# Performance work log

Measured on AMD Instinct MI355X. Metric: run time of the kernel, lower is better.

Reference implementation:

```python
import jax, jax.numpy as jnp
from jax import lax
import numpy as np

B, T, H, L = 4096, 7, 512, 256
D = 2 * H  # bidirectional LSTM feature dim


def _lstm(x, wih, whh, bih, bhh, reverse):
    # x: [B, T, L]; torch gate order i, f, g, o
    b, hdim = x.shape[0], whh.shape[0]
    xs = jnp.swapaxes(x, 0, 1)  # [T, B, L]
    bias = bih + bhh

    def step(carry, xt):
        h, c = carry
        gates = xt @ wih + h @ whh + bias
        i, f, g, o = jnp.split(gates, 4, axis=-1)
        c = jax.nn.sigmoid(f) * c + jax.nn.sigmoid(i) * jnp.tanh(g)
        h = jax.nn.sigmoid(o) * jnp.tanh(c)
        return (h, c), h

    h0 = jnp.zeros((b, hdim), x.dtype)
    _, hs = lax.scan(step, (h0, h0), xs, reverse=reverse)
    return jnp.swapaxes(hs, 0, 1)  # [B, T, H]


def _att(enc, dec):
    # Sequential attention: keys/values start as enc and grow with each decoder output.
    keys = enc  # [B, T, D]
    outs = []
    for i in range(dec.shape[1]):  # fixed small T=7, Python loop is static
        q = dec[:, i, :]                                  # [B, D]
        scores = jnp.einsum('bd,btd->bt', q, keys)        # dot over features
        a = jax.nn.softmax(scores, axis=1)
        ctx = jnp.einsum('bt,btd->bd', a, keys)
        out = ctx + q
        outs.append(out)
        keys = jnp.concatenate([keys, out[:, None, :]], axis=1)
    return jnp.stack(outs, axis=1)  # [B, T, D]


def _deconv(x, w, b):
    # torch ConvTranspose2d (stride 1, pad 0) == full conv with flipped, in/out-swapped kernel
    kh, kw = w.shape[2], w.shape[3]
    w2 = jnp.transpose(w[:, :, ::-1, ::-1], (1, 0, 2, 3))  # [out, in, kh, kw]
    y = lax.conv_general_dilated(x, w2, (1, 1), ((kh - 1, kh - 1), (kw - 1, kw - 1)),
                                 dimension_numbers=('NCHW', 'OIHW', 'NCHW'))
    return y + b[None, :, None, None]


def setup_inputs() -> dict:
    key = jax.random.key(0)
    ks = jax.random.split(key, 12)
    p = lambda k, shape: jax.random.normal(k, shape, jnp.float32) * 0.02
    return {
        'lstm_enc': jax.random.normal(ks[0], (B, T, D), jnp.float32),
        'gaussian_noise': jax.random.normal(ks[1], (B, L), jnp.float32),
        'embedrep_w': p(ks[2], (L, L * T)), 'embedrep_b': jnp.zeros((L * T,), jnp.float32),
        'wih_f': p(ks[3], (L, 4 * H)), 'whh_f': p(ks[4], (H, 4 * H)),
        'bih_f': jnp.zeros((4 * H,), jnp.float32), 'bhh_f': jnp.zeros((4 * H,), jnp.float32),
        'wih_b': p(ks[5], (L, 4 * H)), 'whh_b': p(ks[6], (H, 4 * H)),
        'bih_b': jnp.zeros((4 * H,), jnp.float32), 'bhh_b': jnp.zeros((4 * H,), jnp.float32),
        'emb_w': p(ks[7], (D, 1024)), 'emb_b': jnp.zeros((1024,), jnp.float32),
        'dc3_w': p(ks[8], (64, 32, 1, 3)), 'dc3_b': jnp.zeros((32,), jnp.float32),
        'dc1_w': p(ks[9], (32, 16, 1, 5)), 'dc1_b': jnp.zeros((16,), jnp.float32),
        'dc2_w': p(ks[10], (16, 1, 3, 3)), 'dc2_b': jnp.zeros((1,), jnp.float32),
        'infer': 0,
    }


def reference(lstm_enc, gaussian_noise, embedrep_w, embedrep_b,
              wih_f, whh_f, bih_f, bhh_f, wih_b, whh_b, bih_b, bhh_b,
              emb_w, emb_b, dc3_w, dc3_b, dc1_w, dc1_b, dc2_w, dc2_b, infer):
    b = lstm_enc.shape[0]
    g1 = jax.nn.soft_sign(gaussian_noise @ embedrep_w + embedrep_b)   # [B, L*T]
    rep = g1.reshape(b, T, L)                                          # [B, 7, L]
    hf = _lstm(rep, wih_f, whh_f, bih_f, bhh_f, False)
    hb = _lstm(rep, wih_b, whh_b, bih_b, bhh_b, True)
    lstm1 = jnp.concatenate([hf, hb], axis=-1)                         # [B, 7, 2H]
    att_out = _att(lstm_enc, lstm1)                                    # [B, 7, 2H]
    emb = att_out @ emb_w + emb_b                                      # [B, 7, 1024]
    up = jax.nn.soft_sign(emb).reshape(b * T, 64, 1, 16)
    x = jax.nn.leaky_relu(_deconv(up, dc3_w, dc3_b))                   # [B*7, 32, 1, 18]
    x = jax.nn.leaky_relu(_deconv(x, dc1_w, dc1_b))                    # [B*7, 16, 1, 22]
    x = jax.nn.leaky_relu(_deconv(x, dc2_w, dc2_b))                    # [B*7, 1, 3, 24]
    x = jax.nn.softmax(x, axis=2)                                      # softmax over H dim (=3)
    out = x.reshape(b, T, 1, 3, 24)[:, :, -1, :, :]                    # [B, 7, 3, 24]
    return out
```

## Files before the change

### kernel.cpp

```cpp
#include <hip/hip_runtime.h>
#include <stdint.h>


typedef __attribute__((ext_vector_type(4))) float f32x4;
typedef __attribute__((ext_vector_type(8))) short bf16x8;
typedef __attribute__((ext_vector_type(4))) unsigned short us4;

__device__ __forceinline__ unsigned short f2b(float f) {
  union { float f; unsigned u; } x; x.f = f;
  unsigned r = x.u + 0x7FFFu + ((x.u >> 16) & 1u);
  return (unsigned short)(r >> 16);
}
__device__ __forceinline__ float b2f(unsigned short s) {
  union { unsigned u; float f; } x; x.u = ((unsigned)s) << 16; return x.f;
}
__device__ __forceinline__ float sigmoidf(float x) {
  return 1.f / (1.f + __expf(-x));
}
__device__ __forceinline__ float fast_tanh(float x) {
  x = fminf(15.f, fmaxf(-15.f, x));
  float e = __expf(2.f * x);
  return (e - 1.f) / (e + 1.f);
}

__device__ __forceinline__ void gl_lds16(const void* g, void* l) {
  auto gp = reinterpret_cast<const __attribute__((address_space(1))) unsigned int*>(
      reinterpret_cast<uintptr_t>(g));
  auto lp = reinterpret_cast<__attribute__((address_space(3))) unsigned int*>(
      reinterpret_cast<uintptr_t>(l));
  __builtin_amdgcn_global_load_lds(gp, lp, 16, 0, 0);
}


__device__ __forceinline__ void stage128x32(const unsigned short* src, int ld,
                                            unsigned short* hbase, int tid) {
  const int row_in = tid >> 2;
  const int gidx = tid & 3;
#pragma unroll
  for (int r = 0; r < 2; ++r) {
    int row = r * 64 + row_in;
    int gsrc = gidx ^ ((row >> 1) & 3);
    gl_lds16(src + (size_t)row * ld + gsrc * 8, hbase + r * 2048 + (tid >> 6) * 512);
  }
}

__device__ __forceinline__ bf16x8 lds_fragH(const unsigned short* hbase, int row, int lq) {
  return *(const bf16x8*)(hbase + row * 32 + (lq ^ (((row >> 1) & 3) << 3)));
}

__device__ __forceinline__ void tile16(const unsigned short* Ab, const unsigned short* Bb,
                                       int wm, int wn, int lane, f32x4 (&acc)[4][4]) {
  const int lr = lane & 15, lq = (lane >> 4) * 8;
  bf16x8 a[4], b[4];
#pragma unroll
  for (int i = 0; i < 4; ++i) a[i] = lds_fragH(Ab, wm * 64 + i * 16 + lr, lq);
#pragma unroll
  for (int n = 0; n < 4; ++n) b[n] = lds_fragH(Bb, wn * 64 + n * 16 + lr, lq);
  __builtin_amdgcn_s_setprio(1);
#pragma unroll
  for (int i = 0; i < 4; ++i)
#pragma unroll
    for (int n = 0; n < 4; ++n)
      acc[i][n] = __builtin_amdgcn_mfma_f32_16x16x32_bf16(a[i], b[n], acc[i][n], 0, 0, 0);
  __builtin_amdgcn_s_setprio(0);
}

#define R3TOP(t, NT)                                                      \
  if ((t) + 1 < (NT)) asm volatile("s_waitcnt vmcnt(4)" ::: "memory");    \
  else                asm volatile("s_waitcnt vmcnt(0)" ::: "memory");    \
  __builtin_amdgcn_s_barrier();                                           \
  __builtin_amdgcn_sched_barrier(0);

__device__ __forceinline__ void stage128x64(const unsigned short* src, int ld,
                                            unsigned short* lds, int wv, int lane) {
#pragma unroll
  for (int r = 0; r < 4; ++r) {
    int row = r * 32 + wv * 8 + (lane >> 3);
    gl_lds16(src + (size_t)row * ld + (lane & 7) * 8, lds + (r * 32 + wv * 8) * 64);
  }
}
__device__ __forceinline__ void mfma_tile(const unsigned short* As, const unsigned short* Bs,
                                          int wm, int wn, int lane, f32x4 acc[4][4]) {
#pragma unroll
  for (int kk = 0; kk < 2; ++kk) {
    int ko = kk * 32 + (lane >> 4) * 8;
    bf16x8 a[4], b[4];
#pragma unroll
    for (int i = 0; i < 4; ++i)
      a[i] = *(const bf16x8*)(As + (size_t)(wm * 64 + i * 16 + (lane & 15)) * 64 + ko);
#pragma unroll
    for (int i = 0; i < 4; ++i)
      b[i] = *(const bf16x8*)(Bs + (size_t)(wn * 64 + i * 16 + (lane & 15)) * 64 + ko);
#pragma unroll
    for (int mi = 0; mi < 4; ++mi)
#pragma unroll
      for (int ni = 0; ni < 4; ++ni)
        acc[mi][ni] = __builtin_amdgcn_mfma_f32_16x16x32_bf16(a[mi], b[ni], acc[mi][ni], 0, 0, 0);
  }
}

__global__ __launch_bounds__(256) void pack_kernel(
    const float* __restrict__ noise, const float* __restrict__ erep_w,
    const float* __restrict__ emb_w,
    const float* __restrict__ wih_f, const float* __restrict__ whh_f,
    const float* __restrict__ bih_f, const float* __restrict__ bhh_f,
    const float* __restrict__ wih_b, const float* __restrict__ whh_b,
    const float* __restrict__ bih_b, const float* __restrict__ bhh_b,
    unsigned short* __restrict__ noiseb, unsigned short* __restrict__ erepT,
    unsigned short* __restrict__ embT, unsigned short* __restrict__ lstmW,
    float* __restrict__ lstmB) {
  const int N0 = 4096 * 256;
  const int N1 = 1792 * 256;
  const int N2 = 1024 * 1024;
  const int N3 = 2 * 2048 * 768;
  const int N4 = 2 * 2048;
  const int total = N0 + N1 + N2 + N3 + N4;
  for (int i = blockIdx.x * 256 + threadIdx.x; i < total; i += gridDim.x * 256) {
    int x = i;
    if (x < N0) { noiseb[x] = f2b(noise[x]); continue; }
    x -= N0;
    if (x < N1) { int n = x >> 8, k = x & 255; erepT[x] = f2b(erep_w[k * 1792 + n]); continue; }
    x -= N1;
    if (x < N2) {
      int n = x >> 10, k = x & 1023;
      int o = (n & 63) * 16 + (n >> 6);
      embT[x] = f2b(emb_w[k * 1024 + o]);
      continue;
    }
    x -= N2;
    if (x < N3) {
      int dir = x / (2048 * 768);
      int r = x - dir * (2048 * 768);
      int npk = r / 768, k = r - (r / 768) * 768;
      int blk = npk >> 6, g = (npk >> 4) & 3, u = npk & 15;
      int o = g * 512 + blk * 16 + u;
      const float* wih = dir ? wih_b : wih_f;
      const float* whh = dir ? whh_b : whh_f;
      float v = (k < 256) ? wih[k * 2048 + o] : whh[(k - 256) * 2048 + o];
      lstmW[x] = f2b(v);
      continue;
    }
    x -= N3;
    {
      int dir = x >> 11, npk = x & 2047;
      int blk = npk >> 6, g = (npk >> 4) & 3, u = npk & 15;
      int o = g * 512 + blk * 16 + u;
      lstmB[x] = dir ? (bih_b[o] + bhh_b[o]) : (bih_f[o] + bhh_f[o]);
    }
  }
}

__global__ __launch_bounds__(256) void gemm_rep_kernel(
    const unsigned short* __restrict__ A, const unsigned short* __restrict__ Bt,
    const float* __restrict__ bias, unsigned short* __restrict__ rep_t) {
  __shared__ unsigned short As[128 * 64];
  __shared__ unsigned short Bs[128 * 64];
  const int lane = threadIdx.x & 63, wv = threadIdx.x >> 6;
  const int wm = wv >> 1, wn = wv & 1;
  const int m0 = blockIdx.y * 128, n0 = blockIdx.x * 128;
  f32x4 acc[4][4];
#pragma unroll
  for (int i = 0; i < 4; ++i)
#pragma unroll
    for (int j = 0; j < 4; ++j) acc[i][j] = (f32x4){0.f, 0.f, 0.f, 0.f};
  for (int k0 = 0; k0 < 256; k0 += 64) {
    stage128x64(A + (size_t)m0 * 256 + k0, 256, As, wv, lane);
    stage128x64(Bt + (size_t)n0 * 256 + k0, 256, Bs, wv, lane);
    __syncthreads();
    mfma_tile(As, Bs, wm, wn, lane, acc);
    __syncthreads();
  }
#pragma unroll
  for (int ni = 0; ni < 4; ++ni) {
    int n = n0 + wn * 64 + ni * 16 + (lane & 15);
    float bv = bias[n];
    int t = n >> 8, l = n & 255;
#pragma unroll
    for (int mi = 0; mi < 4; ++mi)
#pragma unroll
      for (int r = 0; r < 4; ++r) {
        int m = m0 + wm * 64 + mi * 16 + (lane >> 4) * 4 + r;
        float v = acc[mi][ni][r] + bv;
        v = v / (1.f + fabsf(v));
        rep_t[((size_t)t * 4096 + m) * 256 + l] = f2b(v);
      }
  }
}

__global__ __launch_bounds__(256, 3) void lstm_step128_kernel(
    const unsigned short* __restrict__ rep_t, const unsigned short* __restrict__ Wp,
    const float* __restrict__ biasP, unsigned short* __restrict__ hbuf,
    unsigned short* __restrict__ cbuf, unsigned short* __restrict__ lstm1, int step) {
  __shared__ unsigned short Ar[3][4096];
  __shared__ unsigned short Br[3][4096];
  const int tid = threadIdx.x, lane = tid & 63, wv = tid >> 6;
  const int wm = wv >> 1, wn = wv & 1;
  const int swz = (blockIdx.x & 7) * 128 + (blockIdx.x >> 3);
  const int dir = swz >> 9;
  const int rem = swz & 511;
  const int by = rem >> 4, bx = rem & 15;
  const int m0 = by * 128, n0 = bx * 128;
  const int t_proc = dir ? (6 - step) : step;
  const unsigned short* W = Wp + (size_t)dir * 2048 * 768;
  const unsigned short* hin = hbuf + ((size_t)(step & 1) * 2 + dir) * (4096 * 512);
  unsigned short* hout = hbuf + ((size_t)((step + 1) & 1) * 2 + dir) * (4096 * 512);
  unsigned short* cp = cbuf + (size_t)dir * (4096 * 512);
  const unsigned short* xsrc = rep_t + (size_t)t_proc * 4096 * 256;

  f32x4 acc[4][4];
#pragma unroll
  for (int i = 0; i < 4; ++i)
#pragma unroll
    for (int j = 0; j < 4; ++j) acc[i][j] = (f32x4){0.f, 0.f, 0.f, 0.f};

  auto asrc = [&](int tt) {
    return tt < 8 ? xsrc + (size_t)m0 * 256 + tt * 32
                  : hin + (size_t)m0 * 512 + (tt - 8) * 32;
  };
  auto ald = [&](int tt) { return tt < 8 ? 256 : 512; };

  stage128x32(asrc(0), ald(0), Ar[0], tid);
  stage128x32(W + (size_t)n0 * 768 + 0 * 32, 768, Br[0], tid);
  stage128x32(asrc(1), ald(1), Ar[1], tid);
  stage128x32(W + (size_t)n0 * 768 + 1 * 32, 768, Br[1], tid);

#pragma unroll
  for (int t = 0; t < 24; ++t) {
    R3TOP(t, 24)
    if (t + 2 < 24) {
      stage128x32(asrc(t + 2), ald(t + 2), Ar[(t + 2) % 3], tid);
      stage128x32(W + (size_t)n0 * 768 + (t + 2) * 32, 768, Br[(t + 2) % 3], tid);
    }
    tile16(Ar[t % 3], Br[t % 3], wm, wn, lane, acc);
  }

  const int u = lane & 15;
  const int blk = (n0 + wn * 64) >> 6;
  const int j = blk * 16 + u;
  const float bz0 = biasP[dir * 2048 + blk * 64 + 0 * 16 + u];
  const float bz1 = biasP[dir * 2048 + blk * 64 + 1 * 16 + u];
  const float bz2 = biasP[dir * 2048 + blk * 64 + 2 * 16 + u];
  const float bz3 = biasP[dir * 2048 + blk * 64 + 3 * 16 + u];
#pragma unroll
  for (int mi = 0; mi < 4; ++mi)
#pragma unroll
    for (int r = 0; r < 4; ++r) {
      int row = m0 + wm * 64 + mi * 16 + (lane >> 4) * 4 + r;
      float gi = acc[mi][0][r] + bz0;
      float gf = acc[mi][1][r] + bz1;
      float gg = acc[mi][2][r] + bz2;
      float go = acc[mi][3][r] + bz3;
      size_t ci = (size_t)row * 512 + j;
      float c = sigmoidf(gf) * b2f(cp[ci]) + sigmoidf(gi) * fast_tanh(gg);
      cp[ci] = f2b(c);
      float h = sigmoidf(go) * fast_tanh(c);
      unsigned short hb = f2b(h);
      hout[ci] = hb;
      lstm1[((size_t)row * 7 + t_proc) * 1024 + dir * 512 + j] = hb;
    }
}

__global__ __launch_bounds__(256) void att_fused3_kernel(
    const float* __restrict__ enc, const unsigned short* __restrict__ lstm1,
    unsigned short* __restrict__ att) {
  __shared__ unsigned short Qs[7 * 1032];
  __shared__ unsigned short Es[7 * 1032];
  __shared__ float P[8 * 256];
  __shared__ float sG[98];
  __shared__ float sC[7][14];
  __shared__ float sA[16];
  const int tid = threadIdx.x, lane = tid & 63, wv = tid >> 6;
  const int b = blockIdx.x;
  const float* Eb = enc + (size_t)b * 7168;
  const unsigned short* Qb = lstm1 + (size_t)b * 7168;

  if (tid < 98) ((float*)sC)[tid] = 0.f;

  const f32x4* Eb4 = (const f32x4*)Eb;
  const int d0 = tid * 4;
#pragma unroll
  for (int r = 0; r < 7; ++r) {
    f32x4 v = Eb4[r * 256 + tid];
    us4 hi;
#pragma unroll
    for (int e = 0; e < 4; ++e) hi[e] = f2b(v[e]);
    *(us4*)&Es[r * 1032 + d0] = hi;
    *(us4*)&Qs[r * 1032 + d0] = *(const us4*)(Qb + r * 1024 + d0);
  }
  asm volatile("s_waitcnt lgkmcnt(0)" ::: "memory");
  __builtin_amdgcn_sched_barrier(0);

  {
    const int rr = lane & 15;
    const int rowc = rr % 7;
    const int kbase = wv * 256 + (lane >> 4) * 8;
    f32x4 g1 = {0.f, 0.f, 0.f, 0.f}, g2 = {0.f, 0.f, 0.f, 0.f};
#pragma unroll
    for (int s = 0; s < 8; ++s) {
      const int k0 = kbase + s * 32;
      bf16x8 aq = *(const bf16x8*)&Qs[rowc * 1032 + k0];
      bf16x8 be = *(const bf16x8*)&Es[rowc * 1032 + k0];
      g1 = __builtin_amdgcn_mfma_f32_16x16x32_bf16(aq, be, g1, 0, 0, 0);
      g2 = __builtin_amdgcn_mfma_f32_16x16x32_bf16(aq, aq, g2, 0, 0, 0);
    }
    *(f32x4*)&P[((wv * 2 + 0) * 64 + lane) * 4] = g1;
    *(f32x4*)&P[((wv * 2 + 1) * 64 + lane) * 4] = g2;
  }
  __syncthreads();

  if (tid < 98) {
    int i = tid / 14, v = tid - i * 14;
    int col = v < 7 ? v : v - 7;
    int tile = v < 7 ? 0 : 1;
    int ln = ((i >> 2) << 4) | col;
    int rg = i & 3;
    float s = 0.f;
#pragma unroll
    for (int w = 0; w < 4; ++w) s += P[((w * 2 + tile) * 64 + ln) * 4 + rg];
    sG[i * 14 + v] = s;
  }
  __syncthreads();
  if (wv == 0) {
    for (int i = 0; i < 7; ++i) {
      const int nt = 7 + i;
      float s = -1e30f;
      if (lane < 7) {
        s = sG[i * 14 + lane];
      } else if (lane < nt) {
        int jj = lane - 7;
        float a2 = 0.f;
#pragma unroll
        for (int v = 0; v < 14; ++v) a2 += sC[jj][v] * sG[i * 14 + v];
        s = a2;
      }
      float mx = s;
#pragma unroll
      for (int off = 8; off >= 1; off >>= 1) mx = fmaxf(mx, __shfl_xor(mx, off, 16));
      float e = (lane < nt) ? __expf(s - mx) : 0.f;
      float sum = e;
#pragma unroll
      for (int off = 8; off >= 1; off >>= 1) sum += __shfl_xor(sum, off, 16);
      float aw = e / sum;
      if (lane < 16) sA[lane] = aw;
      if (lane < 14) {
        float c = (lane < 7) ? sA[lane] : 0.f;
        for (int jj = 0; jj < i; ++jj) c += sA[7 + jj] * sC[jj][lane];
        if (lane == 7 + i) c += 1.f;
        sC[i][lane] = c;
      }
    }
  }
  __syncthreads();

  {
    float acc[7][4];
#pragma unroll
    for (int i = 0; i < 7; ++i)
#pragma unroll
      for (int e = 0; e < 4; ++e) acc[i][e] = 0.f;
#pragma unroll
    for (int t = 0; t < 7; ++t) {
      us4 ev = *(const us4*)&Es[t * 1032 + d0];
      float evf[4];
#pragma unroll
      for (int e = 0; e < 4; ++e) evf[e] = b2f(ev[e]);
#pragma unroll
      for (int i = 0; i < 7; ++i) {
        float c = sC[i][t];
#pragma unroll
        for (int e = 0; e < 4; ++e) acc[i][e] += c * evf[e];
      }
    }
#pragma unroll
    for (int m = 0; m < 7; ++m) {
      us4 qv = *(const us4*)&Qs[m * 1032 + d0];
      float qf[4];
#pragma unroll
      for (int e = 0; e < 4; ++e) qf[e] = b2f(qv[e]);
#pragma unroll
      for (int i = m; i < 7; ++i) {
        float c = sC[i][7 + m];
#pragma unroll
        for (int e = 0; e < 4; ++e) acc[i][e] += c * qf[e];
      }
    }
    unsigned short* Ab = att + (size_t)b * 7168;
#pragma unroll
    for (int i = 0; i < 7; ++i) {
      us4 r;
#pragma unroll
      for (int e = 0; e < 4; ++e) r[e] = f2b(acc[i][e]);
      *(us4*)(Ab + i * 1024 + d0) = r;
    }
  }
}

__global__ __launch_bounds__(256, 3) void gemm_emb128_kernel(
    const unsigned short* __restrict__ A, const unsigned short* __restrict__ Bt,
    const float* __restrict__ bias, unsigned short* __restrict__ up_t) {
  __shared__ unsigned short Ar[3][4096];
  __shared__ unsigned short Br[3][4096];
  const int tid = threadIdx.x, lane = tid & 63, wv = tid >> 6;
  const int wm = wv >> 1, wn = wv & 1;
  const int swz = (blockIdx.x & 7) * 224 + (blockIdx.x >> 3);
  const int by = swz >> 3, bx = swz & 7;
  const int m0 = by * 128, n0 = bx * 128;

  f32x4 acc[4][4];
#pragma unroll
  for (int i = 0; i < 4; ++i)
#pragma unroll
    for (int j = 0; j < 4; ++j) acc[i][j] = (f32x4){0.f, 0.f, 0.f, 0.f};

  const unsigned short* Abase = A + (size_t)m0 * 1024;
  const unsigned short* Bbase = Bt + (size_t)n0 * 1024;

  stage128x32(Abase + 0 * 32, 1024, Ar[0], tid);
  stage128x32(Bbase + 0 * 32, 1024, Br[0], tid);
  stage128x32(Abase + 1 * 32, 1024, Ar[1], tid);
  stage128x32(Bbase + 1 * 32, 1024, Br[1], tid);

#pragma unroll
  for (int t = 0; t < 32; ++t) {
    R3TOP(t, 32)
    if (t + 2 < 32) {
      stage128x32(Abase + (t + 2) * 32, 1024, Ar[(t + 2) % 3], tid);
      stage128x32(Bbase + (t + 2) * 32, 1024, Br[(t + 2) % 3], tid);
    }
    tile16(Ar[t % 3], Br[t % 3], wm, wn, lane, acc);
  }

#pragma unroll
  for (int ni = 0; ni < 4; ++ni) {
    int np = n0 + wn * 64 + ni * 16 + (lane & 15);
    int o = (np & 63) * 16 + (np >> 6);
    float bv = bias[o];
#pragma unroll
    for (int mi = 0; mi < 4; ++mi)
#pragma unroll
      for (int r = 0; r < 4; ++r) {
        int m = m0 + wm * 64 + mi * 16 + (lane >> 4) * 4 + r;
        float v = acc[mi][ni][r] + bv;
        v = v / (1.f + fabsf(v));
        up_t[(size_t)m * 1024 + np] = f2b(v);
      }
  }
}

__global__ __launch_bounds__(256) void dc3_kernel(const unsigned short* __restrict__ up_t,
                                                  const float* __restrict__ w3,
                                                  const float* __restrict__ b3,
                                                  unsigned short* __restrict__ y1_t) {
  const int lane = threadIdx.x & 63, wv = threadIdx.x >> 6;
  const int kq = (lane >> 4) * 8;
  const int oc = lane & 15;
  bf16x8 bf[2][6];
#pragma unroll
  for (int nt = 0; nt < 2; ++nt)
#pragma unroll
    for (int kk = 0; kk < 6; ++kk) {
      bf16x8 v;
#pragma unroll
      for (int t = 0; t < 8; ++t) {
        int k = kk * 32 + kq + t;
        int jj = k >> 6, ic = k & 63;
        v[t] = (short)f2b(w3[((size_t)ic * 32 + nt * 16 + oc) * 3 + jj]);
      }
      bf[nt][kk] = v;
    }
  const float bia0 = b3[oc], bia1 = b3[16 + oc];
  const int base_chunk = blockIdx.x * 32 + wv * 8;
  for (int cc = 0; cc < 8; ++cc) {
    const int chunk = base_chunk + cc;
    int m = chunk * 16 + (lane & 15);
    int img = m / 18, ow = m - img * 18;
    const unsigned short* arow = up_t + (size_t)img * 1024;
    f32x4 acc0 = {0.f, 0.f, 0.f, 0.f}, acc1 = {0.f, 0.f, 0.f, 0.f};
#pragma unroll
    for (int kk = 0; kk < 6; ++kk) {
      int jj = kk >> 1;
      int ic0 = (kk & 1) * 32 + kq;
      int iw = ow - jj;
      bf16x8 a = {0, 0, 0, 0, 0, 0, 0, 0};
      if ((unsigned)iw < 16u) a = *(const bf16x8*)(arow + iw * 64 + ic0);
      acc0 = __builtin_amdgcn_mfma_f32_16x16x32_bf16(a, bf[0][kk], acc0, 0, 0, 0);
      acc1 = __builtin_amdgcn_mfma_f32_16x16x32_bf16(a, bf[1][kk], acc1, 0, 0, 0);
    }
#pragma unroll
    for (int r = 0; r < 4; ++r) {
      int mm = chunk * 16 + (lane >> 4) * 4 + r;
      float v0 = acc0[r] + bia0; v0 = v0 > 0.f ? v0 : 0.01f * v0;
      float v1 = acc1[r] + bia1; v1 = v1 > 0.f ? v1 : 0.01f * v1;
      y1_t[(size_t)mm * 32 + oc] = f2b(v0);
      y1_t[(size_t)mm * 32 + 16 + oc] = f2b(v1);
    }
  }
}

__global__ __launch_bounds__(256) void dc1_kernel(const unsigned short* __restrict__ y1_t,
                                                  const float* __restrict__ w1,
                                                  const float* __restrict__ b1,
                                                  unsigned short* __restrict__ y2_t) {
  const int lane = threadIdx.x & 63, wv = threadIdx.x >> 6;
  const int kq = (lane >> 4) * 8;
  const int oc = lane & 15;
  bf16x8 bf[5];
#pragma unroll
  for (int kk = 0; kk < 5; ++kk) {
    bf16x8 v;
#pragma unroll
    for (int t = 0; t < 8; ++t) {
      int ic = kq + t;
      v[t] = (short)f2b(w1[((size_t)ic * 16 + oc) * 5 + kk]);
    }
    bf[kk] = v;
  }
  const float bia = b1[oc];
  const int base_chunk = blockIdx.x * 32 + wv * 8;
  for (int cc = 0; cc < 8; ++cc) {
    const int chunk = base_chunk + cc;
    int m = chunk * 16 + (lane & 15);
    int img = m / 22, ow = m - img * 22;
    const unsigned short* abase = y1_t + (size_t)img * 18 * 32;
    f32x4 acc = {0.f, 0.f, 0.f, 0.f};
#pragma unroll
    for (int kk = 0; kk < 5; ++kk) {
      int iw = ow - kk;
      bf16x8 a = {0, 0, 0, 0, 0, 0, 0, 0};
      if ((unsigned)iw < 18u) a = *(const bf16x8*)(abase + iw * 32 + kq);
      acc = __builtin_amdgcn_mfma_f32_16x16x32_bf16(a, bf[kk], acc, 0, 0, 0);
    }
#pragma unroll
    for (int r = 0; r < 4; ++r) {
      int mm = chunk * 16 + (lane >> 4) * 4 + r;
      float v = acc[r] + bia;
      v = v > 0.f ? v : 0.01f * v;
      y2_t[(size_t)mm * 16 + oc] = f2b(v);
    }
  }
}

__global__ __launch_bounds__(256) void dc2_kernel(const unsigned short* __restrict__ y2_t,
                                                  const float* __restrict__ w2,
                                                  const float* __restrict__ b2,
                                                  float* __restrict__ out) {
  int idx = blockIdx.x * 256 + threadIdx.x;
  int img = idx / 24, ow = idx - img * 24;
  float lg0 = b2[0], lg1 = b2[0], lg2 = b2[0];
#pragma unroll
  for (int jj = 0; jj < 3; ++jj) {
    int iw = ow - jj;
    if ((unsigned)iw >= 22u) continue;
    const unsigned short* row = y2_t + ((size_t)img * 22 + iw) * 16;
    bf16x8 v0 = *(const bf16x8*)(row);
    bf16x8 v1 = *(const bf16x8*)(row + 8);
    float x[16];
#pragma unroll
    for (int ic = 0; ic < 8; ++ic) {
      x[ic] = b2f((unsigned short)v0[ic]);
      x[8 + ic] = b2f((unsigned short)v1[ic]);
    }
#pragma unroll
    for (int ic = 0; ic < 16; ++ic) {
      lg0 += x[ic] * w2[ic * 9 + 0 * 3 + jj];
      lg1 += x[ic] * w2[ic * 9 + 1 * 3 + jj];
      lg2 += x[ic] * w2[ic * 9 + 2 * 3 + jj];
    }
  }
  lg0 = lg0 > 0.f ? lg0 : 0.01f * lg0;
  lg1 = lg1 > 0.f ? lg1 : 0.01f * lg1;
  lg2 = lg2 > 0.f ? lg2 : 0.01f * lg2;
  float mx = fmaxf(lg0, fmaxf(lg1, lg2));
  float e0 = __expf(lg0 - mx), e1 = __expf(lg1 - mx), e2 = __expf(lg2 - mx);
  float inv = 1.f / (e0 + e1 + e2);
  size_t ob = (size_t)img * 72 + ow;
  out[ob] = e0 * inv;
  out[ob + 24] = e1 * inv;
  out[ob + 48] = e2 * inv;
}

extern "C" void kernel_launch(void* const* d_in, const int* in_sizes, int n_in,
                              void* d_out, int out_size, void* d_ws, size_t ws_size,
                              hipStream_t stream) {
  (void)in_sizes; (void)n_in; (void)out_size; (void)ws_size;
  const float* enc    = (const float*)d_in[0];
  const float* noise  = (const float*)d_in[1];
  const float* erep_w = (const float*)d_in[2];
  const float* erep_b = (const float*)d_in[3];
  const float* wih_f  = (const float*)d_in[4];
  const float* whh_f  = (const float*)d_in[5];
  const float* bih_f  = (const float*)d_in[6];
  const float* bhh_f  = (const float*)d_in[7];
  const float* wih_b  = (const float*)d_in[8];
  const float* whh_b  = (const float*)d_in[9];
  const float* bih_b  = (const float*)d_in[10];
  const float* bhh_b  = (const float*)d_in[11];
  const float* emb_w  = (const float*)d_in[12];
  const float* emb_b  = (const float*)d_in[13];
  const float* dc3w   = (const float*)d_in[14];
  const float* dc3b   = (const float*)d_in[15];
  const float* dc1w   = (const float*)d_in[16];
  const float* dc1b   = (const float*)d_in[17];
  const float* dc2w   = (const float*)d_in[18];
  const float* dc2b   = (const float*)d_in[19];
  float* out = (float*)d_out;

  char* p = (char*)d_ws;
  auto carve = [&p](size_t bytes) {
    char* r = p;
    p += (bytes + 255) & ~(size_t)255;
    return r;
  };
  unsigned short* rep_t  = (unsigned short*)carve(7ull * 4096 * 256 * 2);
  unsigned short* lstmW  = (unsigned short*)carve(2ull * 2048 * 768 * 2);
  float*          lstmB  = (float*)carve(2ull * 2048 * 4);
  unsigned short* noiseb = (unsigned short*)carve(4096ull * 256 * 2);
  unsigned short* erepT  = (unsigned short*)carve(1792ull * 256 * 2);
  unsigned short* embT   = (unsigned short*)carve(1024ull * 1024 * 2);
  unsigned short* hbuf   = (unsigned short*)carve(4ull * 4096 * 512 * 2);
  unsigned short* cbuf   = (unsigned short*)carve(2ull * 4096 * 512 * 2);
  unsigned short* lstm1  = (unsigned short*)carve(4096ull * 7 * 1024 * 2);
  unsigned short* att    = (unsigned short*)carve(28672ull * 1024 * 2);
  unsigned short* up_t   = (unsigned short*)carve(28672ull * 1024 * 2);
  unsigned short* y1_t   = (unsigned short*)carve(28672ull * 18 * 32 * 2);
  unsigned short* y2_t   = (unsigned short*)carve(28672ull * 22 * 16 * 2);

  hipMemsetAsync(hbuf, 0, 2ull * 4096 * 512 * 2, stream);
  hipMemsetAsync(cbuf, 0, 2ull * 4096 * 512 * 2, stream);

  pack_kernel<<<2048, 256, 0, stream>>>(noise, erep_w, emb_w, wih_f, whh_f, bih_f, bhh_f,
                                        wih_b, whh_b, bih_b, bhh_b,
                                        noiseb, erepT, embT, lstmW, lstmB);
  gemm_rep_kernel<<<dim3(14, 32), 256, 0, stream>>>(noiseb, erepT, erep_b, rep_t);
  for (int s = 0; s < 7; ++s)
    lstm_step128_kernel<<<1024, 256, 0, stream>>>(rep_t, lstmW, lstmB, hbuf, cbuf, lstm1, s);
  att_fused3_kernel<<<4096, 256, 0, stream>>>(enc, lstm1, att);
  gemm_emb128_kernel<<<1792, 256, 0, stream>>>(att, embT, emb_b, up_t);
  dc3_kernel<<<1008, 256, 0, stream>>>(up_t, dc3w, dc3b, y1_t);
  dc1_kernel<<<1232, 256, 0, stream>>>(y1_t, dc1w, dc1b, y2_t);
  dc2_kernel<<<2688, 256, 0, stream>>>(y2_t, dc2w, dc2b, out);
}
```

Measured before the change: 502.2 us.

## Fuse three deconv kernels via LDS and switch GEMMs to double buffering

Merges the dc3, dc1 and dc2 deconvolution kernels into one kernel. Each block handles 32 images and keeps the intermediate activations in LDS, so the y1/y2 global round trips and two launches go away. Separately, the LSTM step and embedding GEMM kernels move from a three-stage LDS pipeline with partial vmcnt waits to a two-stage double buffer with a full wait each iteration. That halves the tile LDS footprint to allow higher occupancy, but it exposes more load latency per iteration.

```diff
diff --git a/kernel.cpp b/kernel.cpp
--- a/kernel.cpp
+++ b/kernel.cpp
@@ -65,10 +65,9 @@
   __builtin_amdgcn_s_setprio(0);
 }
 
-#define R3TOP(t, NT)                                                      \
-  if ((t) + 1 < (NT)) asm volatile("s_waitcnt vmcnt(4)" ::: "memory");    \
-  else                asm volatile("s_waitcnt vmcnt(0)" ::: "memory");    \
-  __builtin_amdgcn_s_barrier();                                           \
+#define DBUF_SYNC()                                   \
+  asm volatile("s_waitcnt vmcnt(0)" ::: "memory");    \
+  __builtin_amdgcn_s_barrier();                       \
   __builtin_amdgcn_sched_barrier(0);
 
 __device__ __forceinline__ void stage128x64(const unsigned short* src, int ld,
@@ -187,12 +186,12 @@
   }
 }
 
-__global__ __launch_bounds__(256, 3) void lstm_step128_kernel(
+__global__ __launch_bounds__(256, 4) void lstm_step128_kernel(
     const unsigned short* __restrict__ rep_t, const unsigned short* __restrict__ Wp,
     const float* __restrict__ biasP, unsigned short* __restrict__ hbuf,
     unsigned short* __restrict__ cbuf, unsigned short* __restrict__ lstm1, int step) {
-  __shared__ unsigned short Ar[3][4096];
-  __shared__ unsigned short Br[3][4096];
+  __shared__ unsigned short Ar[2][4096];
+  __shared__ unsigned short Br[2][4096];
   const int tid = threadIdx.x, lane = tid & 63, wv = tid >> 6;
   const int wm = wv >> 1, wn = wv & 1;
   const int swz = (blockIdx.x & 7) * 128 + (blockIdx.x >> 3);
@@ -221,17 +220,16 @@
 
   stage128x32(asrc(0), ald(0), Ar[0], tid);
   stage128x32(W + (size_t)n0 * 768 + 0 * 32, 768, Br[0], tid);
-  stage128x32(asrc(1), ald(1), Ar[1], tid);
-  stage128x32(W + (size_t)n0 * 768 + 1 * 32, 768, Br[1], tid);
+  DBUF_SYNC()
 
 #pragma unroll
   for (int t = 0; t < 24; ++t) {
-    R3TOP(t, 24)
-    if (t + 2 < 24) {
-      stage128x32(asrc(t + 2), ald(t + 2), Ar[(t + 2) % 3], tid);
-      stage128x32(W + (size_t)n0 * 768 + (t + 2) * 32, 768, Br[(t + 2) % 3], tid);
-    }
-    tile16(Ar[t % 3], Br[t % 3], wm, wn, lane, acc);
+    if (t + 1 < 24) {
+      stage128x32(asrc(t + 1), ald(t + 1), Ar[(t + 1) & 1], tid);
+      stage128x32(W + (size_t)n0 * 768 + (t + 1) * 32, 768, Br[(t + 1) & 1], tid);
+    }
+    tile16(Ar[t & 1], Br[t & 1], wm, wn, lane, acc);
+    if (t + 1 < 24) { DBUF_SYNC() }
   }
 
   const int u = lane & 15;
@@ -395,11 +393,11 @@
   }
 }
 
-__global__ __launch_bounds__(256, 3) void gemm_emb128_kernel(
+__global__ __launch_bounds__(256, 5) void gemm_emb128_kernel(
     const unsigned short* __restrict__ A, const unsigned short* __restrict__ Bt,
     const float* __restrict__ bias, unsigned short* __restrict__ up_t) {
-  __shared__ unsigned short Ar[3][4096];
-  __shared__ unsigned short Br[3][4096];
+  __shared__ unsigned short Ar[2][4096];
+  __shared__ unsigned short Br[2][4096];
   const int tid = threadIdx.x, lane = tid & 63, wv = tid >> 6;
   const int wm = wv >> 1, wn = wv & 1;
   const int swz = (blockIdx.x & 7) * 224 + (blockIdx.x >> 3);
@@ -417,17 +415,16 @@
 
   stage128x32(Abase + 0 * 32, 1024, Ar[0], tid);
   stage128x32(Bbase + 0 * 32, 1024, Br[0], tid);
-  stage128x32(Abase + 1 * 32, 1024, Ar[1], tid);
-  stage128x32(Bbase + 1 * 32, 1024, Br[1], tid);
+  DBUF_SYNC()
 
 #pragma unroll
   for (int t = 0; t < 32; ++t) {
-    R3TOP(t, 32)
-    if (t + 2 < 32) {
-      stage128x32(Abase + (t + 2) * 32, 1024, Ar[(t + 2) % 3], tid);
-      stage128x32(Bbase + (t + 2) * 32, 1024, Br[(t + 2) % 3], tid);
-    }
-    tile16(Ar[t % 3], Br[t % 3], wm, wn, lane, acc);
+    if (t + 1 < 32) {
+      stage128x32(Abase + (t + 1) * 32, 1024, Ar[(t + 1) & 1], tid);
+      stage128x32(Bbase + (t + 1) * 32, 1024, Br[(t + 1) & 1], tid);
+    }
+    tile16(Ar[t & 1], Br[t & 1], wm, wn, lane, acc);
+    if (t + 1 < 32) { DBUF_SYNC() }
   }
 
 #pragma unroll
@@ -447,136 +444,132 @@
   }
 }
 
-__global__ __launch_bounds__(256) void dc3_kernel(const unsigned short* __restrict__ up_t,
-                                                  const float* __restrict__ w3,
-                                                  const float* __restrict__ b3,
-                                                  unsigned short* __restrict__ y1_t) {
-  const int lane = threadIdx.x & 63, wv = threadIdx.x >> 6;
+__global__ __launch_bounds__(256) void dc_fused_kernel(
+    const unsigned short* __restrict__ up_t,
+    const float* __restrict__ w3, const float* __restrict__ b3,
+    const float* __restrict__ w1, const float* __restrict__ b1,
+    const float* __restrict__ w2, const float* __restrict__ b2,
+    float* __restrict__ out) {
+  __shared__ unsigned short y1L[576 * 40];
+  __shared__ unsigned short y2L[704 * 24];
+  const int tid = threadIdx.x, lane = tid & 63, wv = tid >> 6;
+  const int g0 = blockIdx.x * 32;
   const int kq = (lane >> 4) * 8;
   const int oc = lane & 15;
-  bf16x8 bf[2][6];
-#pragma unroll
-  for (int nt = 0; nt < 2; ++nt)
-#pragma unroll
-    for (int kk = 0; kk < 6; ++kk) {
+
+  {
+    bf16x8 bf[2][6];
+#pragma unroll
+    for (int nt = 0; nt < 2; ++nt)
+#pragma unroll
+      for (int kk = 0; kk < 6; ++kk) {
+        bf16x8 v;
+#pragma unroll
+        for (int t = 0; t < 8; ++t) {
+          int k = kk * 32 + kq + t;
+          int jj = k >> 6, ic = k & 63;
+          v[t] = (short)f2b(w3[((size_t)ic * 32 + nt * 16 + oc) * 3 + jj]);
+        }
+        bf[nt][kk] = v;
+      }
+    const float bia0 = b3[oc], bia1 = b3[16 + oc];
+    for (int c = wv; c < 36; c += 4) {
+      int m = c * 16 + (lane & 15);
+      int imgl = m / 18, ow = m - imgl * 18;
+      const unsigned short* arow = up_t + (size_t)(g0 + imgl) * 1024;
+      f32x4 acc0 = {0.f, 0.f, 0.f, 0.f}, acc1 = {0.f, 0.f, 0.f, 0.f};
+#pragma unroll
+      for (int kk = 0; kk < 6; ++kk) {
+        int jj = kk >> 1;
+        int ic0 = (kk & 1) * 32 + kq;
+        int iw = ow - jj;
+        bf16x8 a = {0, 0, 0, 0, 0, 0, 0, 0};
+        if ((unsigned)iw < 16u) a = *(const bf16x8*)(arow + iw * 64 + ic0);
+        acc0 = __builtin_amdgcn_mfma_f32_16x16x32_bf16(a, bf[0][kk], acc0, 0, 0, 0);
+        acc1 = __builtin_amdgcn_mfma_f32_16x16x32_bf16(a, bf[1][kk], acc1, 0, 0, 0);
+      }
+#pragma unroll
+      for (int r = 0; r < 4; ++r) {
+        int mm = c * 16 + (lane >> 4) * 4 + r;
+        float v0 = acc0[r] + bia0; v0 = v0 > 0.f ? v0 : 0.01f * v0;
+        float v1 = acc1[r] + bia1; v1 = v1 > 0.f ? v1 : 0.01f * v1;
+        y1L[mm * 40 + oc] = f2b(v0);
+        y1L[mm * 40 + 16 + oc] = f2b(v1);
+      }
+    }
+  }
+  __syncthreads();
+
+  {
+    bf16x8 bf[5];
+#pragma unroll
+    for (int kk = 0; kk < 5; ++kk) {
       bf16x8 v;
 #pragma unroll
       for (int t = 0; t < 8; ++t) {
-        int k = kk * 32 + kq + t;
-        int jj = k >> 6, ic = k & 63;
-        v[t] = (short)f2b(w3[((size_t)ic * 32 + nt * 16 + oc) * 3 + jj]);
-      }
-      bf[nt][kk] = v;
-    }
-  const float bia0 = b3[oc], bia1 = b3[16 + oc];
-  const int base_chunk = blockIdx.x * 32 + wv * 8;
-  for (int cc = 0; cc < 8; ++cc) {
-    const int chunk = base_chunk + cc;
-    int m = chunk * 16 + (lane & 15);
-    int img = m / 18, ow = m - img * 18;
-    const unsigned short* arow = up_t + (size_t)img * 1024;
-    f32x4 acc0 = {0.f, 0.f, 0.f, 0.f}, acc1 = {0.f, 0.f, 0.f, 0.f};
-#pragma unroll
-    for (int kk = 0; kk < 6; ++kk) {
-      int jj = kk >> 1;
-      int ic0 = (kk & 1) * 32 + kq;
+        int ic = kq + t;
+        v[t] = (short)f2b(w1[((size_t)ic * 16 + oc) * 5 + kk]);
+      }
+      bf[kk] = v;
+    }
+    const float bia = b1[oc];
+    for (int c = wv; c < 44; c += 4) {
+      int m = c * 16 + (lane & 15);
+      int imgl = m / 22, ow = m - imgl * 22;
+      const unsigned short* abase = y1L + imgl * (18 * 40);
+      f32x4 acc = {0.f, 0.f, 0.f, 0.f};
+#pragma unroll
+      for (int kk = 0; kk < 5; ++kk) {
+        int iw = ow - kk;
+        bf16x8 a = {0, 0, 0, 0, 0, 0, 0, 0};
+        if ((unsigned)iw < 18u) a = *(const bf16x8*)(abase + iw * 40 + kq);
+        acc = __builtin_amdgcn_mfma_f32_16x16x32_bf16(a, bf[kk], acc, 0, 0, 0);
+      }
+#pragma unroll
+      for (int r = 0; r < 4; ++r) {
+        int mm = c * 16 + (lane >> 4) * 4 + r;
+        float v = acc[r] + bia;
+        v = v > 0.f ? v : 0.01f * v;
+        y2L[mm * 24 + oc] = f2b(v);
+      }
+    }
+  }
+  __syncthreads();
+
+  for (int ii = tid; ii < 768; ii += 256) {
+    int imgl = ii / 24, ow = ii - imgl * 24;
+    float lg0 = b2[0], lg1 = b2[0], lg2 = b2[0];
+#pragma unroll
+    for (int jj = 0; jj < 3; ++jj) {
       int iw = ow - jj;
-      bf16x8 a = {0, 0, 0, 0, 0, 0, 0, 0};
-      if ((unsigned)iw < 16u) a = *(const bf16x8*)(arow + iw * 64 + ic0);
-      acc0 = __builtin_amdgcn_mfma_f32_16x16x32_bf16(a, bf[0][kk], acc0, 0, 0, 0);
-      acc1 = __builtin_amdgcn_mfma_f32_16x16x32_bf16(a, bf[1][kk], acc1, 0, 0, 0);
-    }
-#pragma unroll
-    for (int r = 0; r < 4; ++r) {
-      int mm = chunk * 16 + (lane >> 4) * 4 + r;
-      float v0 = acc0[r] + bia0; v0 = v0 > 0.f ? v0 : 0.01f * v0;
-      float v1 = acc1[r] + bia1; v1 = v1 > 0.f ? v1 : 0.01f * v1;
-      y1_t[(size_t)mm * 32 + oc] = f2b(v0);
-      y1_t[(size_t)mm * 32 + 16 + oc] = f2b(v1);
-    }
-  }
-}
-
-__global__ __launch_bounds__(256) void dc1_kernel(const unsigned short* __restrict__ y1_t,
-                                                  const float* __restrict__ w1,
-                                                  const float* __restrict__ b1,
-                                                  unsigned short* __restrict__ y2_t) {
-  const int lane = threadIdx.x & 63, wv = threadIdx.x >> 6;
-  const int kq = (lane >> 4) * 8;
-  const int oc = lane & 15;
-  bf16x8 bf[5];
-#pragma unroll
-  for (int kk = 0; kk < 5; ++kk) {
-    bf16x8 v;
-#pragma unroll
-    for (int t = 0; t < 8; ++t) {
-      int ic = kq + t;
-      v[t] = (short)f2b(w1[((size_t)ic * 16 + oc) * 5 + kk]);
-    }
-    bf[kk] = v;
-  }
-  const float bia = b1[oc];
-  const int base_chunk = blockIdx.x * 32 + wv * 8;
-  for (int cc = 0; cc < 8; ++cc) {
-    const int chunk = base_chunk + cc;
-    int m = chunk * 16 + (lane & 15);
-    int img = m / 22, ow = m - img * 22;
-    const unsigned short* abase = y1_t + (size_t)img * 18 * 32;
-    f32x4 acc = {0.f, 0.f, 0.f, 0.f};
-#pragma unroll
-    for (int kk = 0; kk < 5; ++kk) {
-      int iw = ow - kk;
-      bf16x8 a = {0, 0, 0, 0, 0, 0, 0, 0};
-      if ((unsigned)iw < 18u) a = *(const bf16x8*)(abase + iw * 32 + kq);
-      acc = __builtin_amdgcn_mfma_f32_16x16x32_bf16(a, bf[kk], acc, 0, 0, 0);
-    }
-#pragma unroll
-    for (int r = 0; r < 4; ++r) {
-      int mm = chunk * 16 + (lane >> 4) * 4 + r;
-      float v = acc[r] + bia;
-      v = v > 0.f ? v : 0.01f * v;
-      y2_t[(size_t)mm * 16 + oc] = f2b(v);
-    }
-  }
-}
-
-__global__ __launch_bounds__(256) void dc2_kernel(const unsigned short* __restrict__ y2_t,
-                                                  const float* __restrict__ w2,
-                                                  const float* __restrict__ b2,
-                                                  float* __restrict__ out) {
-  int idx = blockIdx.x * 256 + threadIdx.x;
-  int img = idx / 24, ow = idx - img * 24;
-  float lg0 = b2[0], lg1 = b2[0], lg2 = b2[0];
-#pragma unroll
-  for (int jj = 0; jj < 3; ++jj) {
-    int iw = ow - jj;
-    if ((unsigned)iw >= 22u) continue;
-    const unsigned short* row = y2_t + ((size_t)img * 22 + iw) * 16;
-    bf16x8 v0 = *(const bf16x8*)(row);
-    bf16x8 v1 = *(const bf16x8*)(row + 8);
-    float x[16];
-#pragma unroll
-    for (int ic = 0; ic < 8; ++ic) {
-      x[ic] = b2f((unsigned short)v0[ic]);
-      x[8 + ic] = b2f((unsigned short)v1[ic]);
-    }
-#pragma unroll
-    for (int ic = 0; ic < 16; ++ic) {
-      lg0 += x[ic] * w2[ic * 9 + 0 * 3 + jj];
-      lg1 += x[ic] * w2[ic * 9 + 1 * 3 + jj];
-      lg2 += x[ic] * w2[ic * 9 + 2 * 3 + jj];
-    }
-  }
-  lg0 = lg0 > 0.f ? lg0 : 0.01f * lg0;
-  lg1 = lg1 > 0.f ? lg1 : 0.01f * lg1;
-  lg2 = lg2 > 0.f ? lg2 : 0.01f * lg2;
-  float mx = fmaxf(lg0, fmaxf(lg1, lg2));
-  float e0 = __expf(lg0 - mx), e1 = __expf(lg1 - mx), e2 = __expf(lg2 - mx);
-  float inv = 1.f / (e0 + e1 + e2);
-  size_t ob = (size_t)img * 72 + ow;
-  out[ob] = e0 * inv;
-  out[ob + 24] = e1 * inv;
-  out[ob + 48] = e2 * inv;
+      if ((unsigned)iw >= 22u) continue;
+      const unsigned short* row = y2L + (imgl * 22 + iw) * 24;
+      bf16x8 v0 = *(const bf16x8*)(row);
+      bf16x8 v1 = *(const bf16x8*)(row + 8);
+      float x[16];
+#pragma unroll
+      for (int ic = 0; ic < 8; ++ic) {
+        x[ic] = b2f((unsigned short)v0[ic]);
+        x[8 + ic] = b2f((unsigned short)v1[ic]);
+      }
+#pragma unroll
+      for (int ic = 0; ic < 16; ++ic) {
+        lg0 += x[ic] * w2[ic * 9 + 0 * 3 + jj];
+        lg1 += x[ic] * w2[ic * 9 + 1 * 3 + jj];
+        lg2 += x[ic] * w2[ic * 9 + 2 * 3 + jj];
+      }
+    }
+    lg0 = lg0 > 0.f ? lg0 : 0.01f * lg0;
+    lg1 = lg1 > 0.f ? lg1 : 0.01f * lg1;
+    lg2 = lg2 > 0.f ? lg2 : 0.01f * lg2;
+    float mx = fmaxf(lg0, fmaxf(lg1, lg2));
+    float e0 = __expf(lg0 - mx), e1 = __expf(lg1 - mx), e2 = __expf(lg2 - mx);
+    float inv = 1.f / (e0 + e1 + e2);
+    size_t ob = (size_t)(g0 + imgl) * 72 + ow;
+    out[ob] = e0 * inv;
+    out[ob + 24] = e1 * inv;
+    out[ob + 48] = e2 * inv;
+  }
 }
 
 extern "C" void kernel_launch(void* const* d_in, const int* in_sizes, int n_in,
@@ -622,8 +615,6 @@
   unsigned short* lstm1  = (unsigned short*)carve(4096ull * 7 * 1024 * 2);
   unsigned short* att    = (unsigned short*)carve(28672ull * 1024 * 2);
   unsigned short* up_t   = (unsigned short*)carve(28672ull * 1024 * 2);
-  unsigned short* y1_t   = (unsigned short*)carve(28672ull * 18 * 32 * 2);
-  unsigned short* y2_t   = (unsigned short*)carve(28672ull * 22 * 16 * 2);
 
   hipMemsetAsync(hbuf, 0, 2ull * 4096 * 512 * 2, stream);
   hipMemsetAsync(cbuf, 0, 2ull * 4096 * 512 * 2, stream);
@@ -636,7 +627,5 @@
     lstm_step128_kernel<<<1024, 256, 0, stream>>>(rep_t, lstmW, lstmB, hbuf, cbuf, lstm1, s);
   att_fused3_kernel<<<4096, 256, 0, stream>>>(enc, lstm1, att);
   gemm_emb128_kernel<<<1792, 256, 0, stream>>>(att, embT, emb_b, up_t);
-  dc3_kernel<<<1008, 256, 0, stream>>>(up_t, dc3w, dc3b, y1_t);
-  dc1_kernel<<<1232, 256, 0, stream>>>(y1_t, dc1w, dc1b, y2_t);
-  dc2_kernel<<<2688, 256, 0, stream>>>(y2_t, dc2w, dc2b, out);
-}
+  dc_fused_kernel<<<896, 256, 0, stream>>>(up_t, dc3w, dc3b, dc1w, dc1b, dc2w, dc2b, out);
+}
```

After: 682.1 us. 35.8% more time.
